# Performance work log

Hardware: AMD Instinct MI355X
Metric: run time of the kernel (lower is better)

## Reference

```python
import jax, jax.numpy as jnp
import numpy as np

B = 2          # batch size
T2 = 9         # temporal groups (b*t2 = grid_sample batch)
T3 = 27        # t1 // t2
T1 = 243       # t2 * t3
P = 17         # joints
K2 = 9         # kernel_size ** 2
C = 128        # dim_img
CH = [48, 96, 192, 384]
HW = [(96, 72), (48, 36), (24, 18), (12, 9)]
ALPHA = 0.9


def setup_inputs() -> dict:
    key = jax.random.key(0)
    ks = jax.random.split(key, 16)
    inp = {}
    N = B * T2
    for i, (c, (h, w)) in enumerate(zip(CH, HW)):
        inp[f"f{i}"] = jax.random.normal(ks[i], (N, c, h, w), jnp.float32)
    inp["query"] = jax.random.normal(ks[4], (B, T1, P * K2, C), jnp.float32)
    # key holds normalized grid coords in [-1, 1]
    inp["key"] = jax.random.uniform(ks[5], (N, T3, P * K2, 2), jnp.float32) * 2.0 - 1.0
    inp["value"] = jax.random.normal(ks[6], (B, T1, P, C), jnp.float32)
    s = 0.05
    inp["w_off"] = jax.random.normal(ks[7], (2, C), jnp.float32) * s
    inp["b_off"] = jnp.zeros((2,), jnp.float32)
    inp["w_attn"] = jax.random.normal(ks[8], (2, C), jnp.float32) * s
    inp["b_attn"] = jnp.zeros((2,), jnp.float32)
    for i, c in enumerate(CH):
        inp[f"we{i}"] = jax.random.normal(ks[9 + i], (C, c), jnp.float32) * s
        inp[f"be{i}"] = jnp.zeros((C,), jnp.float32)
    inp["conv_w"] = jax.random.normal(ks[13], (C, C, K2), jnp.float32) * s
    inp["conv_b"] = jnp.zeros((C,), jnp.float32)
    return inp


def _grid_sample(img, grid):
    """Bilinear grid_sample, align_corners=False, zero padding.
    img: [N, C, H, W]; grid: [N, Hg, Wg, 2] in [-1,1] (x=width, y=height).
    Returns [N, Hg, Wg, C] (channels-last for the following 1x1 conv)."""
    N, Cin, H, W = img.shape
    gx, gy = grid[..., 0], grid[..., 1]
    ix = ((gx + 1.0) * W - 1.0) * 0.5
    iy = ((gy + 1.0) * H - 1.0) * 0.5
    ix0 = jnp.floor(ix); iy0 = jnp.floor(iy)
    wx1 = ix - ix0; wx0 = 1.0 - wx1
    wy1 = iy - iy0; wy0 = 1.0 - wy1
    bidx = jnp.arange(N)[:, None, None]

    def gather(yy, xx):
        yi = yy.astype(jnp.int32); xi = xx.astype(jnp.int32)
        valid = (yi >= 0) & (yi < H) & (xi >= 0) & (xi < W)
        yc = jnp.clip(yi, 0, H - 1); xc = jnp.clip(xi, 0, W - 1)
        v = img[bidx, :, yc, xc]  # [N, Hg, Wg, C]
        return v * valid[..., None].astype(img.dtype)

    out = (gather(iy0, ix0) * (wy0 * wx0)[..., None]
           + gather(iy0, ix0 + 1.0) * (wy0 * wx1)[..., None]
           + gather(iy0 + 1.0, ix0) * (wy1 * wx0)[..., None]
           + gather(iy0 + 1.0, ix0 + 1.0) * (wy1 * wx1)[..., None])
    return out


def reference(f0, f1, f2, f3, query, key, value,
              w_off, b_off, w_attn, b_attn,
              we0, be0, we1, be1, we2, be2, we3, be3,
              conv_w, conv_b):
    b, t1, p, c = value.shape            # [B, 243, 17, 128]
    t3 = key.shape[1]                    # 27
    t2 = t1 // t3                        # 9

    # learned offsets per query location, squashed by tanh
    off = jnp.tanh(jnp.einsum('btqc,oc->btqo', query, w_off) + b_off)   # [b,t1,153,2]
    # per-joint softmax weights, tiled over the k^2 kernel taps
    aw = jax.nn.softmax(jnp.einsum('btpc,oc->btpo', value, w_attn) + b_attn, axis=-1)  # [b,t1,17,2]
    aw = jnp.tile(aw, (1, 1, K2, 1))                                     # [b,t1,153,2]

    sp = (off * aw).reshape(b * t2, t3, p * K2, 2)
    sampling_positions = key + sp                                        # [b*t2, 27, 153, 2]

    fmaps = (f0, f1, f2, f3)
    ws = (we0, we1, we2, we3)
    bs = (be0, be1, be2, be3)
    feats = []
    for f, w, bb in zip(fmaps, ws, bs):
        g = _grid_sample(f, sampling_positions)                          # [b*t2, 27, 153, C_in]
        e = jnp.einsum('nhwc,oc->nhwo', g, w) + bb                        # 1x1 conv embed -> 128
        feats.append(e.reshape(b, t2 * t3, p * K2, C))                    # [b, 243, 153, 128]
    new_query = jnp.mean(jnp.stack(feats, axis=-2), axis=-2)             # fuse 4 levels
    new_query = (1.0 - ALPHA) * new_query + ALPHA * query

    # grouped-by-position conv1d over the k^2 taps (full-width kernel -> length 1)
    x = new_query.reshape(b, t1, p, K2, c)                               # 'b t (p k) c'
    new_value = jnp.einsum('btpkc,ock->btpo', x, conv_w) + conv_b        # [b, 243, 17, 128]
    return (new_query, new_value, sampling_positions)
```

## Files before the change

kernel.cpp:

```cpp
#include <hip/hip_runtime.h>
#include <hip/hip_bf16.h>

static constexpr int NQ_SIZE = 9517824;
static constexpr int NV_SIZE = 1057536;
static constexpr int NPOS    = 74358;
static constexpr int M_CONV  = 8262;

static constexpr long E0_OFF = 0;
static constexpr long E1_OFF = 15925248;
static constexpr long E2_OFF = E1_OFF + 3981312;
static constexpr long E3_OFF = E2_OFF + 995328;
static constexpr long E_END  = E3_OFF + 248832;

static constexpr int SEG_AW = 65;
static constexpr int SEG_L3 = SEG_AW + 18;
static constexpr int SEG_L2 = SEG_L3 + 72;
static constexpr int SEG_L1 = SEG_L2 + 252;
static constexpr int SEG_L0 = SEG_L1 + 972;
static constexpr int SEG_CT = SEG_L0 + 576;
static constexpr int PREP_GRID = SEG_CT;

typedef __attribute__((ext_vector_type(8))) short short8;
typedef __attribute__((ext_vector_type(4))) float floatx4;

__device__ __forceinline__ float bf2f(unsigned short u) {
    union { unsigned int i; float f; } v; v.i = ((unsigned)u) << 16; return v.f;
}
__device__ __forceinline__ unsigned short f2bf_rne(float f) {
    union { float f; unsigned int i; } v; v.f = f;
    unsigned int u = v.i;
    u += 0x7fffu + ((u >> 16) & 1u);
    return (unsigned short)(u >> 16);
}
__device__ __forceinline__ short8 pack8(const float* t) {
    union { unsigned short u[8]; short8 s; } r;
    #pragma unroll
    for (int i = 0; i < 8; ++i) r.u[i] = f2bf_rne(t[i]);
    return r.s;
}

template<int K, int M, bool FULLM>
__device__ __forceinline__ void proj_body(
    const float* __restrict__ A, const float* __restrict__ W,
    unsigned short* __restrict__ Eo, int m0, int tid,
    unsigned short (*Bs)[104])
{
    constexpr int KC      = (K < 96) ? K : 96;
    constexpr int KCPAD   = (KC + 31) & ~31;
    constexpr int KT      = KCPAD / 32;
    constexpr int NCH     = K / KC;
    constexpr bool NEEDPAD = (KCPAD != KC);

    const int lane = tid & 63;
    const int wave = tid >> 6;
    const int l15  = lane & 15;
    const int quad = lane >> 4;
    const int mg0  = m0 + wave * 32 + l15;
    const int mg1  = mg0 + 16;
    const bool v0  = FULLM || (mg0 < M);
    const bool v1  = FULLM || (mg1 < M);

    floatx4 acc[2][8];
    #pragma unroll
    for (int f = 0; f < 2; ++f)
        #pragma unroll
        for (int nt = 0; nt < 8; ++nt) acc[f][nt] = (floatx4){0.f, 0.f, 0.f, 0.f};

    const int so  = tid >> 1;
    const int skb = (tid & 1) * (KCPAD / 2);

    #pragma unroll 1
    for (int ch = 0; ch < NCH; ++ch) {
        const int kc = ch * KC;

        float bt[KCPAD / 2];
        {
            const float* wp = W + (long)so * K + kc + skb;
            #pragma unroll
            for (int j = 0; j < KCPAD / 2; ++j) {
                bt[j] = 0.f;
                if (!NEEDPAD || (skb + j < KC)) bt[j] = wp[j];
            }
        }

        float a0[KT][8], a1[KT][8];
        #pragma unroll
        for (int kt = 0; kt < KT; ++kt) {
            const int kg = kc + kt * 32 + quad * 8;
            const float* ap = A + (long)kg * M + mg0;
            if (FULLM && (!NEEDPAD || (kg + 8 <= K))) {
                #pragma unroll
                for (int j = 0; j < 8; ++j) {
                    a0[kt][j] = ap[(long)j * M];
                    a1[kt][j] = ap[(long)j * M + 16];
                }
            } else {
                #pragma unroll
                for (int j = 0; j < 8; ++j) {
                    a0[kt][j] = 0.f; a1[kt][j] = 0.f;
                    if (kg + j < K) {
                        if (v0) a0[kt][j] = ap[(long)j * M];
                        if (v1) a1[kt][j] = ap[(long)j * M + 16];
                    }
                }
            }
        }

        if (ch) __syncthreads();
        {
            #pragma unroll
            for (int j = 0; j < KCPAD / 2; j += 8) {
                unsigned short u[8];
                #pragma unroll
                for (int i = 0; i < 8; ++i) u[i] = f2bf_rne(bt[j + i]);
                *(uint4*)&Bs[so][skb + j] = *(const uint4*)u;
            }
        }
        __syncthreads();

        #pragma unroll
        for (int kt = 0; kt < KT; ++kt) {
            short8 af0 = pack8(a0[kt]);
            short8 af1 = pack8(a1[kt]);
            #pragma unroll
            for (int nt = 0; nt < 8; ++nt) {
                short8 bf = *(const short8*)&Bs[nt * 16 + l15][kt * 32 + quad * 8];
                acc[0][nt] = __builtin_amdgcn_mfma_f32_16x16x32_bf16(af0, bf, acc[0][nt], 0, 0, 0);
                acc[1][nt] = __builtin_amdgcn_mfma_f32_16x16x32_bf16(af1, bf, acc[1][nt], 0, 0, 0);
            }
        }
    }

    #pragma unroll
    for (int f = 0; f < 2; ++f) {
        const int rb = m0 + wave * 32 + f * 16 + quad * 4;
        #pragma unroll
        for (int nt = 0; nt < 8; ++nt) {
            const int col = nt * 16 + l15;
            #pragma unroll
            for (int r = 0; r < 4; ++r) {
                if (FULLM || (rb + r < M))
                    Eo[(long)(rb + r) * 128 + col] = f2bf_rne(acc[f][nt][r]);
            }
        }
    }
}

__global__ __launch_bounds__(256) void prep_k(
    const float* __restrict__ f0, const float* __restrict__ f1,
    const float* __restrict__ f2, const float* __restrict__ f3,
    const float* __restrict__ we0, const float* __restrict__ we1,
    const float* __restrict__ we2, const float* __restrict__ we3,
    const float* __restrict__ conv_w, unsigned short* __restrict__ convT2,
    const float* __restrict__ value,
    const float* __restrict__ w_attn, const float* __restrict__ b_attn,
    float* __restrict__ awbuf, unsigned short* __restrict__ Ebase)
{
    const int bid = blockIdx.x;
    const int tid = threadIdx.x;

    if (bid < SEG_AW) {
        int t = bid * 256 + tid;
        if (t < 16524) {
            int rp = t >> 1, o = t & 1;
            const float* vrow = value + (long)rp * 128;
            const float* wrow = w_attn + o * 128;
            float s = 0.f;
            for (int c = 0; c < 128; c += 4) {
                float4 v = *(const float4*)(vrow + c);
                float4 w = *(const float4*)(wrow + c);
                s += v.x * w.x + v.y * w.y + v.z * w.z + v.w * w.w;
            }
            s += b_attn[o];
            float so = __shfl_xor(s, 1);
            float m = fmaxf(s, so);
            float e = __expf(s - m), eo = __expf(so - m);
            awbuf[t] = e / (e + eo);
        }
    } else if (bid < SEG_L0) {
        __shared__ unsigned short Bs[128][104];

        if (bid < SEG_L3) {
            int n = bid - SEG_AW;
            proj_body<384, 108, false>(f3 + (long)n * 384 * 108, we3,
                Ebase + E3_OFF + (long)n * 108 * 128, 0, tid, Bs);
        } else if (bid < SEG_L2) {
            int r = bid - SEG_L3; int n = r >> 2, t = r & 3;
            const float* A = f2 + (long)n * 192 * 432;
            unsigned short* Eo = Ebase + E2_OFF + (long)n * 432 * 128;
            if (t < 3) proj_body<192, 432, true >(A, we2, Eo, t * 128, tid, Bs);
            else       proj_body<192, 432, false>(A, we2, Eo, t * 128, tid, Bs);
        } else if (bid < SEG_L1) {
            int r = bid - SEG_L2; int n = r / 14, t = r - n * 14;
            const float* A = f1 + (long)n * 96 * 1728;
            unsigned short* Eo = Ebase + E1_OFF + (long)n * 1728 * 128;
            if (t < 13) proj_body<96, 1728, true >(A, we1, Eo, t * 128, tid, Bs);
            else        proj_body<96, 1728, false>(A, we1, Eo, t * 128, tid, Bs);
        } else {
            int r = bid - SEG_L1; int n = r / 54, t = r - n * 54;
            proj_body<48, 6912, true>(f0 + (long)n * 48 * 6912, we0,
                Ebase + E0_OFF + (long)n * 6912 * 128, t * 128, tid, Bs);
        }
    } else {
        int idx = (bid - SEG_L0) * 256 + tid;
        if (idx < 147456) {
            int o = idx / 1152, kk = idx - o * 1152;
            int k2 = kk >> 7, c = kk & 127;
            convT2[idx] = f2bf_rne(conv_w[o * 1152 + c * 9 + k2]);
        }
    }
}

__global__ __launch_bounds__(256) void gather_k(
    const unsigned short* __restrict__ Ebase,
    const float* __restrict__ query, const float* __restrict__ key,
    const float* __restrict__ w_off, const float* __restrict__ b_off,
    const float* __restrict__ awbuf,
    const float* __restrict__ be0, const float* __restrict__ be1,
    const float* __restrict__ be2, const float* __restrict__ be3,
    float* __restrict__ nq, float* __restrict__ samp)
{
    const int tid = threadIdx.x;
    const int pos = blockIdx.x * 8 + (tid >> 5);
    if (pos >= NPOS) return;
    const int l32 = tid & 31;
    const int c4  = l32 << 2;
    const int bt1 = pos / 153, q = pos - bt1 * 153;
    const int b  = bt1 / 243, t1 = bt1 - b * 243;
    const int t2 = t1 / 27,  t3 = t1 - t2 * 27;
    const int n  = b * 9 + t2;
    const int p  = q % 17;

    const long qi = ((long)bt1 * 153 + q) * 128 + c4;
    const float4 qv = *(const float4*)(query + qi);

    float4 w0 = *(const float4*)(w_off + c4);
    float4 w1 = *(const float4*)(w_off + 128 + c4);
    float s0 = qv.x * w0.x + qv.y * w0.y + qv.z * w0.z + qv.w * w0.w;
    float s1 = qv.x * w1.x + qv.y * w1.y + qv.z * w1.z + qv.w * w1.w;
    #pragma unroll
    for (int m = 16; m >= 1; m >>= 1) {
        s0 += __shfl_xor(s0, m);
        s1 += __shfl_xor(s1, m);
    }
    const float aw0 = awbuf[(bt1 * 17 + p) * 2];
    const float aw1 = awbuf[(bt1 * 17 + p) * 2 + 1];
    const float off0 = tanhf(s0 + b_off[0]);
    const float off1 = tanhf(s1 + b_off[1]);
    const long kidx = (((long)n * 27 + t3) * 153 + q) * 2;
    const float gx = key[kidx]     + off0 * aw0;
    const float gy = key[kidx + 1] + off1 * aw1;
    if (l32 == 0) {
        samp[kidx]     = gx;
        samp[kidx + 1] = gy;
    }

    float ax = 0.f, ay = 0.f, az = 0.f, aww = 0.f;
    const long Eoffs[4] = {E0_OFF, E1_OFF, E2_OFF, E3_OFF};
    const int Hs[4] = {96, 48, 24, 12}, Wd[4] = {72, 36, 18, 9};
    #pragma unroll
    for (int l = 0; l < 4; ++l) {
        const int H = Hs[l], W = Wd[l];
        const unsigned short* E = Ebase + Eoffs[l] + (long)n * H * W * 128 + c4;
        float ix = ((gx + 1.f) * (float)W - 1.f) * 0.5f;
        float iy = ((gy + 1.f) * (float)H - 1.f) * 0.5f;
        float fx0 = floorf(ix), fy0 = floorf(iy);
        int x0 = (int)fx0, y0 = (int)fy0;
        int x1 = x0 + 1, y1 = y0 + 1;
        float wx1 = ix - fx0, wx0 = 1.f - wx1;
        float wy1 = iy - fy0, wy0 = 1.f - wy1;
        float w00 = wy0 * wx0, w01 = wy0 * wx1, w10 = wy1 * wx0, w11 = wy1 * wx1;
        bool vy0 = (unsigned)y0 < (unsigned)H, vy1 = (unsigned)y1 < (unsigned)H;
        bool vx0 = (unsigned)x0 < (unsigned)W, vx1 = (unsigned)x1 < (unsigned)W;
        if (vy0 && vx0) { ushort4 v = *(const ushort4*)(E + ((long)y0 * W + x0) * 128);
            ax = fmaf(w00, bf2f(v.x), ax); ay = fmaf(w00, bf2f(v.y), ay);
            az = fmaf(w00, bf2f(v.z), az); aww = fmaf(w00, bf2f(v.w), aww); }
        if (vy0 && vx1) { ushort4 v = *(const ushort4*)(E + ((long)y0 * W + x1) * 128);
            ax = fmaf(w01, bf2f(v.x), ax); ay = fmaf(w01, bf2f(v.y), ay);
            az = fmaf(w01, bf2f(v.z), az); aww = fmaf(w01, bf2f(v.w), aww); }
        if (vy1 && vx0) { ushort4 v = *(const ushort4*)(E + ((long)y1 * W + x0) * 128);
            ax = fmaf(w10, bf2f(v.x), ax); ay = fmaf(w10, bf2f(v.y), ay);
            az = fmaf(w10, bf2f(v.z), az); aww = fmaf(w10, bf2f(v.w), aww); }
        if (vy1 && vx1) { ushort4 v = *(const ushort4*)(E + ((long)y1 * W + x1) * 128);
            ax = fmaf(w11, bf2f(v.x), ax); ay = fmaf(w11, bf2f(v.y), ay);
            az = fmaf(w11, bf2f(v.z), az); aww = fmaf(w11, bf2f(v.w), aww); }
    }
    float bsx = be0[c4]     + be1[c4]     + be2[c4]     + be3[c4];
    float bsy = be0[c4 + 1] + be1[c4 + 1] + be2[c4 + 1] + be3[c4 + 1];
    float bsz = be0[c4 + 2] + be1[c4 + 2] + be2[c4 + 2] + be3[c4 + 2];
    float bsw = be0[c4 + 3] + be1[c4 + 3] + be2[c4 + 3] + be3[c4 + 3];
    float mx = 0.25f * (ax + bsx), my = 0.25f * (ay + bsy);
    float mz = 0.25f * (az + bsz), mw = 0.25f * (aww + bsw);
    float4 o;
    o.x = 0.1f * mx + 0.9f * qv.x;
    o.y = 0.1f * my + 0.9f * qv.y;
    o.z = 0.1f * mz + 0.9f * qv.z;
    o.w = 0.1f * mw + 0.9f * qv.w;
    *(float4*)(nq + qi) = o;
}

__global__ __launch_bounds__(256) void conv_mfma_k(
    const float* __restrict__ nq, const unsigned short* __restrict__ convT2,
    const float* __restrict__ conv_b, float* __restrict__ nv)
{
    __shared__ unsigned short As[32][72];
    __shared__ unsigned short Bs[64][72];

    const int tid  = threadIdx.x;
    const int lane = tid & 63;
    const int wave = tid >> 6;
    const int wm = (wave & 1) * 16;
    const int wn = (wave >> 1) * 32;
    const int m0 = blockIdx.x * 32;
    const int n0 = blockIdx.y * 64;
    const int l15  = lane & 15;
    const int quad = lane >> 4;

    floatx4 acc[2];
    acc[0] = (floatx4){0.f, 0.f, 0.f, 0.f};
    acc[1] = acc[0];

    const int am = tid >> 3;
    const int ak = (tid & 7) << 3;
    const int bn = tid >> 2;
    const int bk = (tid & 3) << 4;

    float4 a0, a1; uint4 bv0, bv1;
    auto fetch = [&](int k0) {
        a0 = (float4){0,0,0,0}; a1 = a0;
        int row = m0 + am;
        if (row < M_CONV) {
            a0 = *(const float4*)(nq + (long)row * 1152 + k0 + ak);
            a1 = *(const float4*)(nq + (long)row * 1152 + k0 + ak + 4);
        }
        bv0 = *(const uint4*)(convT2 + (long)(n0 + bn) * 1152 + k0 + bk);
        bv1 = *(const uint4*)(convT2 + (long)(n0 + bn) * 1152 + k0 + bk + 8);
    };
    fetch(0);

    for (int k0 = 0; k0 < 1152; k0 += 64) {
        unsigned short t[8] = {f2bf_rne(a0.x), f2bf_rne(a0.y), f2bf_rne(a0.z), f2bf_rne(a0.w),
                               f2bf_rne(a1.x), f2bf_rne(a1.y), f2bf_rne(a1.z), f2bf_rne(a1.w)};
        *(uint4*)&As[am][ak] = *(const uint4*)t;
        *(uint4*)&Bs[bn][bk] = bv0;
        *(uint4*)&Bs[bn][bk + 8] = bv1;
        __syncthreads();
        if (k0 + 64 < 1152) fetch(k0 + 64);

        #pragma unroll
        for (int kt = 0; kt < 2; ++kt) {
            short8 af = *(const short8*)&As[wm + l15][kt * 32 + quad * 8];
            #pragma unroll
            for (int nt = 0; nt < 2; ++nt) {
                short8 bf = *(const short8*)&Bs[wn + nt * 16 + l15][kt * 32 + quad * 8];
                acc[nt] = __builtin_amdgcn_mfma_f32_16x16x32_bf16(af, bf, acc[nt], 0, 0, 0);
            }
        }
        __syncthreads();
    }

    #pragma unroll
    for (int nt = 0; nt < 2; ++nt) {
        int col = n0 + wn + nt * 16 + l15;
        float bias = conv_b[col];
        #pragma unroll
        for (int r = 0; r < 4; ++r) {
            int row = m0 + wm + quad * 4 + r;
            if (row < M_CONV)
                nv[(long)row * 128 + col] = acc[nt][r] + bias;
        }
    }
}

extern "C" void kernel_launch(void* const* d_in, const int* in_sizes, int n_in,
                              void* d_out, int out_size, void* d_ws, size_t ws_size,
                              hipStream_t stream) {
    const float* f0     = (const float*)d_in[0];
    const float* f1     = (const float*)d_in[1];
    const float* f2     = (const float*)d_in[2];
    const float* f3     = (const float*)d_in[3];
    const float* query  = (const float*)d_in[4];
    const float* key    = (const float*)d_in[5];
    const float* value  = (const float*)d_in[6];
    const float* w_off  = (const float*)d_in[7];
    const float* b_off  = (const float*)d_in[8];
    const float* w_attn = (const float*)d_in[9];
    const float* b_attn = (const float*)d_in[10];
    const float* we0    = (const float*)d_in[11];
    const float* be0    = (const float*)d_in[12];
    const float* we1    = (const float*)d_in[13];
    const float* be1    = (const float*)d_in[14];
    const float* we2    = (const float*)d_in[15];
    const float* be2    = (const float*)d_in[16];
    const float* we3    = (const float*)d_in[17];
    const float* be3    = (const float*)d_in[18];
    const float* conv_w = (const float*)d_in[19];
    const float* conv_b = (const float*)d_in[20];

    float* out  = (float*)d_out;
    float* nq   = out;
    float* nv   = out + NQ_SIZE;
    float* samp = out + NQ_SIZE + NV_SIZE;

    unsigned short* Ebase  = (unsigned short*)d_ws;
    unsigned short* convT2 = Ebase + E_END;
    float* awbuf = nv;

    prep_k<<<PREP_GRID, 256, 0, stream>>>(
        f0, f1, f2, f3, we0, we1, we2, we3, conv_w, convT2,
        value, w_attn, b_attn, awbuf, Ebase);

    gather_k<<<(NPOS + 7) / 8, 256, 0, stream>>>(
        Ebase, query, key, w_off, b_off, awbuf, be0, be1, be2, be3, nq, samp);

    conv_mfma_k<<<dim3(259, 2), 256, 0, stream>>>(nq, convT2, conv_b, nv);
}
```

Before: 232.8 us.

## Coalesce projection stores, widen gather to 8 channels, precompute bias sum

The projection epilogue now stages the bf16 tile in shared memory and writes it out as coalesced 16-byte rows instead of scattered 2-byte stores. A-operand loads are interleaved per k-step to cut register pressure, and the prep segments are reordered so the heavy projection blocks are scheduled first. The gather kernel uses 16 lanes per position with 8 channels each, branchless clamped 16-byte loads with zeroed weights for out-of-range taps, and a swizzled block index. The summed embedding bias is precomputed once in prep instead of summed per thread. Risks include the larger 32KB shared buffer lowering prep occupancy and the extra loads issued for out-of-bounds corners.

```diff
diff --git a/kernel.cpp b/kernel.cpp
--- a/kernel.cpp
+++ b/kernel.cpp
@@ -12,13 +12,13 @@
 static constexpr long E3_OFF = E2_OFF + 995328;
 static constexpr long E_END  = E3_OFF + 248832;
 
-static constexpr int SEG_AW = 65;
-static constexpr int SEG_L3 = SEG_AW + 18;
+static constexpr int SEG_L3 = 18;
 static constexpr int SEG_L2 = SEG_L3 + 72;
 static constexpr int SEG_L1 = SEG_L2 + 252;
 static constexpr int SEG_L0 = SEG_L1 + 972;
-static constexpr int SEG_CT = SEG_L0 + 576;
-static constexpr int PREP_GRID = SEG_CT;
+static constexpr int SEG_AW = SEG_L0 + 65;
+static constexpr int SEG_CT = SEG_AW + 576;
+static constexpr int PREP_GRID = SEG_CT + 1;
 
 typedef __attribute__((ext_vector_type(8))) short short8;
 typedef __attribute__((ext_vector_type(4))) float floatx4;
@@ -43,13 +43,15 @@
 __device__ __forceinline__ void proj_body(
     const float* __restrict__ A, const float* __restrict__ W,
     unsigned short* __restrict__ Eo, int m0, int tid,
-    unsigned short (*Bs)[104])
+    unsigned short* __restrict__ shbuf)
 {
     constexpr int KC      = (K < 96) ? K : 96;
     constexpr int KCPAD   = (KC + 31) & ~31;
     constexpr int KT      = KCPAD / 32;
     constexpr int NCH     = K / KC;
     constexpr bool NEEDPAD = (KCPAD != KC);
+
+    unsigned short (*Bs)[104] = (unsigned short (*)[104])shbuf;
 
     const int lane = tid & 63;
     const int wave = tid >> 6;
@@ -72,56 +74,47 @@
     #pragma unroll 1
     for (int ch = 0; ch < NCH; ++ch) {
         const int kc = ch * KC;
-
-        float bt[KCPAD / 2];
+        if (ch) __syncthreads();
+
         {
             const float* wp = W + (long)so * K + kc + skb;
             #pragma unroll
-            for (int j = 0; j < KCPAD / 2; ++j) {
-                bt[j] = 0.f;
-                if (!NEEDPAD || (skb + j < KC)) bt[j] = wp[j];
-            }
-        }
-
-        float a0[KT][8], a1[KT][8];
+            for (int j = 0; j < KCPAD / 2; j += 8) {
+                float t8[8];
+                #pragma unroll
+                for (int i = 0; i < 8; ++i)
+                    t8[i] = (!NEEDPAD || (skb + j + i < KC)) ? wp[j + i] : 0.f;
+                unsigned short u[8];
+                #pragma unroll
+                for (int i = 0; i < 8; ++i) u[i] = f2bf_rne(t8[i]);
+                *(uint4*)&Bs[so][skb + j] = *(const uint4*)u;
+            }
+        }
+        __syncthreads();
+
         #pragma unroll
         for (int kt = 0; kt < KT; ++kt) {
             const int kg = kc + kt * 32 + quad * 8;
             const float* ap = A + (long)kg * M + mg0;
+            float a0[8], a1[8];
             if (FULLM && (!NEEDPAD || (kg + 8 <= K))) {
                 #pragma unroll
                 for (int j = 0; j < 8; ++j) {
-                    a0[kt][j] = ap[(long)j * M];
-                    a1[kt][j] = ap[(long)j * M + 16];
+                    a0[j] = ap[(long)j * M];
+                    a1[j] = ap[(long)j * M + 16];
                 }
             } else {
                 #pragma unroll
                 for (int j = 0; j < 8; ++j) {
-                    a0[kt][j] = 0.f; a1[kt][j] = 0.f;
+                    a0[j] = 0.f; a1[j] = 0.f;
                     if (kg + j < K) {
-                        if (v0) a0[kt][j] = ap[(long)j * M];
-                        if (v1) a1[kt][j] = ap[(long)j * M + 16];
+                        if (v0) a0[j] = ap[(long)j * M];
+                        if (v1) a1[j] = ap[(long)j * M + 16];
                     }
                 }
             }
-        }
-
-        if (ch) __syncthreads();
-        {
-            #pragma unroll
-            for (int j = 0; j < KCPAD / 2; j += 8) {
-                unsigned short u[8];
-                #pragma unroll
-                for (int i = 0; i < 8; ++i) u[i] = f2bf_rne(bt[j + i]);
-                *(uint4*)&Bs[so][skb + j] = *(const uint4*)u;
-            }
-        }
-        __syncthreads();
-
-        #pragma unroll
-        for (int kt = 0; kt < KT; ++kt) {
-            short8 af0 = pack8(a0[kt]);
-            short8 af1 = pack8(a1[kt]);
+            short8 af0 = pack8(a0);
+            short8 af1 = pack8(a1);
             #pragma unroll
             for (int nt = 0; nt < 8; ++nt) {
                 short8 bf = *(const short8*)&Bs[nt * 16 + l15][kt * 32 + quad * 8];
@@ -131,18 +124,26 @@
         }
     }
 
+    __syncthreads();
     #pragma unroll
     for (int f = 0; f < 2; ++f) {
-        const int rb = m0 + wave * 32 + f * 16 + quad * 4;
         #pragma unroll
         for (int nt = 0; nt < 8; ++nt) {
-            const int col = nt * 16 + l15;
             #pragma unroll
             for (int r = 0; r < 4; ++r) {
-                if (FULLM || (rb + r < M))
-                    Eo[(long)(rb + r) * 128 + col] = f2bf_rne(acc[f][nt][r]);
-            }
-        }
+                int row = wave * 32 + f * 16 + quad * 4 + r;
+                shbuf[row * 128 + nt * 16 + l15] = f2bf_rne(acc[f][nt][r]);
+            }
+        }
+    }
+    __syncthreads();
+    const uint4* sb4 = (const uint4*)shbuf;
+    uint4* eo4 = (uint4*)(Eo + (long)m0 * 128);
+    #pragma unroll
+    for (int j = 0; j < 8; ++j) {
+        int off16 = wave * 512 + j * 64 + lane;
+        if (FULLM || (m0 + (off16 >> 4) < M))
+            eo4[off16] = sb4[off16];
     }
 }
 
@@ -154,13 +155,39 @@
     const float* __restrict__ conv_w, unsigned short* __restrict__ convT2,
     const float* __restrict__ value,
     const float* __restrict__ w_attn, const float* __restrict__ b_attn,
-    float* __restrict__ awbuf, unsigned short* __restrict__ Ebase)
+    const float* __restrict__ be0, const float* __restrict__ be1,
+    const float* __restrict__ be2, const float* __restrict__ be3,
+    float* __restrict__ awbuf, float* __restrict__ besum,
+    unsigned short* __restrict__ Ebase)
 {
+    __shared__ unsigned short shbuf[128 * 128];
     const int bid = blockIdx.x;
     const int tid = threadIdx.x;
 
-    if (bid < SEG_AW) {
-        int t = bid * 256 + tid;
+    if (bid < SEG_L0) {
+        if (bid < SEG_L3) {
+            int n = bid;
+            proj_body<384, 108, false>(f3 + (long)n * 384 * 108, we3,
+                Ebase + E3_OFF + (long)n * 108 * 128, 0, tid, shbuf);
+        } else if (bid < SEG_L2) {
+            int r = bid - SEG_L3; int n = r >> 2, t = r & 3;
+            const float* A = f2 + (long)n * 192 * 432;
+            unsigned short* Eo = Ebase + E2_OFF + (long)n * 432 * 128;
+            if (t < 3) proj_body<192, 432, true >(A, we2, Eo, t * 128, tid, shbuf);
+            else       proj_body<192, 432, false>(A, we2, Eo, t * 128, tid, shbuf);
+        } else if (bid < SEG_L1) {
+            int r = bid - SEG_L2; int n = r / 14, t = r - n * 14;
+            const float* A = f1 + (long)n * 96 * 1728;
+            unsigned short* Eo = Ebase + E1_OFF + (long)n * 1728 * 128;
+            if (t < 13) proj_body<96, 1728, true >(A, we1, Eo, t * 128, tid, shbuf);
+            else        proj_body<96, 1728, false>(A, we1, Eo, t * 128, tid, shbuf);
+        } else {
+            int r = bid - SEG_L1; int n = r / 54, t = r - n * 54;
+            proj_body<48, 6912, true>(f0 + (long)n * 48 * 6912, we0,
+                Ebase + E0_OFF + (long)n * 6912 * 128, t * 128, tid, shbuf);
+        }
+    } else if (bid < SEG_AW) {
+        int t = (bid - SEG_L0) * 256 + tid;
         if (t < 16524) {
             int rp = t >> 1, o = t & 1;
             const float* vrow = value + (long)rp * 128;
@@ -177,37 +204,16 @@
             float e = __expf(s - m), eo = __expf(so - m);
             awbuf[t] = e / (e + eo);
         }
-    } else if (bid < SEG_L0) {
-        __shared__ unsigned short Bs[128][104];
-
-        if (bid < SEG_L3) {
-            int n = bid - SEG_AW;
-            proj_body<384, 108, false>(f3 + (long)n * 384 * 108, we3,
-                Ebase + E3_OFF + (long)n * 108 * 128, 0, tid, Bs);
-        } else if (bid < SEG_L2) {
-            int r = bid - SEG_L3; int n = r >> 2, t = r & 3;
-            const float* A = f2 + (long)n * 192 * 432;
-            unsigned short* Eo = Ebase + E2_OFF + (long)n * 432 * 128;
-            if (t < 3) proj_body<192, 432, true >(A, we2, Eo, t * 128, tid, Bs);
-            else       proj_body<192, 432, false>(A, we2, Eo, t * 128, tid, Bs);
-        } else if (bid < SEG_L1) {
-            int r = bid - SEG_L2; int n = r / 14, t = r - n * 14;
-            const float* A = f1 + (long)n * 96 * 1728;
-            unsigned short* Eo = Ebase + E1_OFF + (long)n * 1728 * 128;
-            if (t < 13) proj_body<96, 1728, true >(A, we1, Eo, t * 128, tid, Bs);
-            else        proj_body<96, 1728, false>(A, we1, Eo, t * 128, tid, Bs);
-        } else {
-            int r = bid - SEG_L1; int n = r / 54, t = r - n * 54;
-            proj_body<48, 6912, true>(f0 + (long)n * 48 * 6912, we0,
-                Ebase + E0_OFF + (long)n * 6912 * 128, t * 128, tid, Bs);
-        }
-    } else {
-        int idx = (bid - SEG_L0) * 256 + tid;
+    } else if (bid < SEG_CT) {
+        int idx = (bid - SEG_AW) * 256 + tid;
         if (idx < 147456) {
             int o = idx / 1152, kk = idx - o * 1152;
             int k2 = kk >> 7, c = kk & 127;
             convT2[idx] = f2bf_rne(conv_w[o * 1152 + c * 9 + k2]);
         }
+    } else {
+        if (tid < 128)
+            besum[tid] = be0[tid] + be1[tid] + be2[tid] + be3[tid];
     }
 }
 
@@ -215,31 +221,36 @@
     const unsigned short* __restrict__ Ebase,
     const float* __restrict__ query, const float* __restrict__ key,
     const float* __restrict__ w_off, const float* __restrict__ b_off,
-    const float* __restrict__ awbuf,
-    const float* __restrict__ be0, const float* __restrict__ be1,
-    const float* __restrict__ be2, const float* __restrict__ be3,
+    const float* __restrict__ awbuf, const float* __restrict__ besum,
     float* __restrict__ nq, float* __restrict__ samp)
 {
     const int tid = threadIdx.x;
-    const int pos = blockIdx.x * 8 + (tid >> 5);
+    const int li  = (blockIdx.x & 7) * 581 + (blockIdx.x >> 3);
+    const int pos = li * 16 + (tid >> 4);
     if (pos >= NPOS) return;
-    const int l32 = tid & 31;
-    const int c4  = l32 << 2;
+    const int l16 = tid & 15;
+    const int c8  = l16 << 3;
+
     const int bt1 = pos / 153, q = pos - bt1 * 153;
     const int b  = bt1 / 243, t1 = bt1 - b * 243;
     const int t2 = t1 / 27,  t3 = t1 - t2 * 27;
     const int n  = b * 9 + t2;
     const int p  = q % 17;
 
-    const long qi = ((long)bt1 * 153 + q) * 128 + c4;
-    const float4 qv = *(const float4*)(query + qi);
-
-    float4 w0 = *(const float4*)(w_off + c4);
-    float4 w1 = *(const float4*)(w_off + 128 + c4);
-    float s0 = qv.x * w0.x + qv.y * w0.y + qv.z * w0.z + qv.w * w0.w;
-    float s1 = qv.x * w1.x + qv.y * w1.y + qv.z * w1.z + qv.w * w1.w;
-    #pragma unroll
-    for (int m = 16; m >= 1; m >>= 1) {
+    const long qi = (long)pos * 128 + c8;
+    const float4 qv0 = *(const float4*)(query + qi);
+    const float4 qv1 = *(const float4*)(query + qi + 4);
+
+    float4 w0a = *(const float4*)(w_off + c8);
+    float4 w0b = *(const float4*)(w_off + c8 + 4);
+    float4 w1a = *(const float4*)(w_off + 128 + c8);
+    float4 w1b = *(const float4*)(w_off + 128 + c8 + 4);
+    float s0 = qv0.x * w0a.x + qv0.y * w0a.y + qv0.z * w0a.z + qv0.w * w0a.w
+             + qv1.x * w0b.x + qv1.y * w0b.y + qv1.z * w0b.z + qv1.w * w0b.w;
+    float s1 = qv0.x * w1a.x + qv0.y * w1a.y + qv0.z * w1a.z + qv0.w * w1a.w
+             + qv1.x * w1b.x + qv1.y * w1b.y + qv1.z * w1b.z + qv1.w * w1b.w;
+    #pragma unroll
+    for (int m = 8; m >= 1; m >>= 1) {
         s0 += __shfl_xor(s0, m);
         s1 += __shfl_xor(s1, m);
     }
@@ -250,18 +261,17 @@
     const long kidx = (((long)n * 27 + t3) * 153 + q) * 2;
     const float gx = key[kidx]     + off0 * aw0;
     const float gy = key[kidx + 1] + off1 * aw1;
-    if (l32 == 0) {
-        samp[kidx]     = gx;
-        samp[kidx + 1] = gy;
-    }
-
-    float ax = 0.f, ay = 0.f, az = 0.f, aww = 0.f;
+    if (l16 == 0) *(float2*)(samp + kidx) = (float2){gx, gy};
+
+    float acc[8];
+    #pragma unroll
+    for (int j = 0; j < 8; ++j) acc[j] = 0.f;
     const long Eoffs[4] = {E0_OFF, E1_OFF, E2_OFF, E3_OFF};
     const int Hs[4] = {96, 48, 24, 12}, Wd[4] = {72, 36, 18, 9};
     #pragma unroll
     for (int l = 0; l < 4; ++l) {
         const int H = Hs[l], W = Wd[l];
-        const unsigned short* E = Ebase + Eoffs[l] + (long)n * H * W * 128 + c4;
+        const unsigned short* E = Ebase + Eoffs[l] + (long)n * H * W * 128 + c8;
         float ix = ((gx + 1.f) * (float)W - 1.f) * 0.5f;
         float iy = ((gy + 1.f) * (float)H - 1.f) * 0.5f;
         float fx0 = floorf(ix), fy0 = floorf(iy);
@@ -269,34 +279,41 @@
         int x1 = x0 + 1, y1 = y0 + 1;
         float wx1 = ix - fx0, wx0 = 1.f - wx1;
         float wy1 = iy - fy0, wy0 = 1.f - wy1;
-        float w00 = wy0 * wx0, w01 = wy0 * wx1, w10 = wy1 * wx0, w11 = wy1 * wx1;
         bool vy0 = (unsigned)y0 < (unsigned)H, vy1 = (unsigned)y1 < (unsigned)H;
         bool vx0 = (unsigned)x0 < (unsigned)W, vx1 = (unsigned)x1 < (unsigned)W;
-        if (vy0 && vx0) { ushort4 v = *(const ushort4*)(E + ((long)y0 * W + x0) * 128);
-            ax = fmaf(w00, bf2f(v.x), ax); ay = fmaf(w00, bf2f(v.y), ay);
-            az = fmaf(w00, bf2f(v.z), az); aww = fmaf(w00, bf2f(v.w), aww); }
-        if (vy0 && vx1) { ushort4 v = *(const ushort4*)(E + ((long)y0 * W + x1) * 128);
-            ax = fmaf(w01, bf2f(v.x), ax); ay = fmaf(w01, bf2f(v.y), ay);
-            az = fmaf(w01, bf2f(v.z), az); aww = fmaf(w01, bf2f(v.w), aww); }
-        if (vy1 && vx0) { ushort4 v = *(const ushort4*)(E + ((long)y1 * W + x0) * 128);
-            ax = fmaf(w10, bf2f(v.x), ax); ay = fmaf(w10, bf2f(v.y), ay);
-            az = fmaf(w10, bf2f(v.z), az); aww = fmaf(w10, bf2f(v.w), aww); }
-        if (vy1 && vx1) { ushort4 v = *(const ushort4*)(E + ((long)y1 * W + x1) * 128);
-            ax = fmaf(w11, bf2f(v.x), ax); ay = fmaf(w11, bf2f(v.y), ay);
-            az = fmaf(w11, bf2f(v.z), az); aww = fmaf(w11, bf2f(v.w), aww); }
-    }
-    float bsx = be0[c4]     + be1[c4]     + be2[c4]     + be3[c4];
-    float bsy = be0[c4 + 1] + be1[c4 + 1] + be2[c4 + 1] + be3[c4 + 1];
-    float bsz = be0[c4 + 2] + be1[c4 + 2] + be2[c4 + 2] + be3[c4 + 2];
-    float bsw = be0[c4 + 3] + be1[c4 + 3] + be2[c4 + 3] + be3[c4 + 3];
-    float mx = 0.25f * (ax + bsx), my = 0.25f * (ay + bsy);
-    float mz = 0.25f * (az + bsz), mw = 0.25f * (aww + bsw);
-    float4 o;
-    o.x = 0.1f * mx + 0.9f * qv.x;
-    o.y = 0.1f * my + 0.9f * qv.y;
-    o.z = 0.1f * mz + 0.9f * qv.z;
-    o.w = 0.1f * mw + 0.9f * qv.w;
-    *(float4*)(nq + qi) = o;
+        float w00 = (vy0 && vx0) ? wy0 * wx0 : 0.f;
+        float w01 = (vy0 && vx1) ? wy0 * wx1 : 0.f;
+        float w10 = (vy1 && vx0) ? wy1 * wx0 : 0.f;
+        float w11 = (vy1 && vx1) ? wy1 * wx1 : 0.f;
+        int yc0 = min(max(y0, 0), H - 1), yc1 = min(max(y1, 0), H - 1);
+        int xc0 = min(max(x0, 0), W - 1), xc1 = min(max(x1, 0), W - 1);
+        short8 v00 = *(const short8*)(E + ((long)yc0 * W + xc0) * 128);
+        short8 v01 = *(const short8*)(E + ((long)yc0 * W + xc1) * 128);
+        short8 v10 = *(const short8*)(E + ((long)yc1 * W + xc0) * 128);
+        short8 v11 = *(const short8*)(E + ((long)yc1 * W + xc1) * 128);
+        #pragma unroll
+        for (int j = 0; j < 8; ++j) {
+            float a = acc[j];
+            a = fmaf(w00, bf2f((unsigned short)v00[j]), a);
+            a = fmaf(w01, bf2f((unsigned short)v01[j]), a);
+            a = fmaf(w10, bf2f((unsigned short)v10[j]), a);
+            a = fmaf(w11, bf2f((unsigned short)v11[j]), a);
+            acc[j] = a;
+        }
+    }
+    const float4 bs0 = *(const float4*)(besum + c8);
+    const float4 bs1 = *(const float4*)(besum + c8 + 4);
+    float4 o0, o1;
+    o0.x = 0.1f * (0.25f * (acc[0] + bs0.x)) + 0.9f * qv0.x;
+    o0.y = 0.1f * (0.25f * (acc[1] + bs0.y)) + 0.9f * qv0.y;
+    o0.z = 0.1f * (0.25f * (acc[2] + bs0.z)) + 0.9f * qv0.z;
+    o0.w = 0.1f * (0.25f * (acc[3] + bs0.w)) + 0.9f * qv0.w;
+    o1.x = 0.1f * (0.25f * (acc[4] + bs1.x)) + 0.9f * qv1.x;
+    o1.y = 0.1f * (0.25f * (acc[5] + bs1.y)) + 0.9f * qv1.y;
+    o1.z = 0.1f * (0.25f * (acc[6] + bs1.z)) + 0.9f * qv1.z;
+    o1.w = 0.1f * (0.25f * (acc[7] + bs1.w)) + 0.9f * qv1.w;
+    *(float4*)(nq + qi)     = o0;
+    *(float4*)(nq + qi + 4) = o1;
 }
 
 __global__ __launch_bounds__(256) void conv_mfma_k(
@@ -405,13 +422,14 @@
     unsigned short* Ebase  = (unsigned short*)d_ws;
     unsigned short* convT2 = Ebase + E_END;
     float* awbuf = nv;
+    float* besum = nv + 16524;
 
     prep_k<<<PREP_GRID, 256, 0, stream>>>(
         f0, f1, f2, f3, we0, we1, we2, we3, conv_w, convT2,
-        value, w_attn, b_attn, awbuf, Ebase);
-
-    gather_k<<<(NPOS + 7) / 8, 256, 0, stream>>>(
-        Ebase, query, key, w_off, b_off, awbuf, be0, be1, be2, be3, nq, samp);
+        value, w_attn, b_attn, be0, be1, be2, be3, awbuf, besum, Ebase);
+
+    gather_k<<<4648, 256, 0, stream>>>(
+        Ebase, query, key, w_off, b_off, awbuf, besum, nq, samp);
 
     conv_mfma_k<<<dim3(259, 2), 256, 0, stream>>>(nq, convT2, conv_b, nv);
 }
```

New measurement: 217.2 us. 6.7% less time.
